# Performance work log

Measured on AMD Instinct MI355X. Metric: run time of the kernel, lower is better.

The kernel has to match this reference:

```python
import jax, jax.numpy as jnp
import numpy as np

NB_POOLS = 256


def setup_inputs() -> dict:
    key = jax.random.key(0)
    x = jax.random.normal(key, (32, 32, 32, 512), dtype=jnp.float32)
    return {"x": x}


def reference(x) -> jnp.ndarray:
    B, R, C, F = x.shape
    nb_maps = R * C
    x3 = x.reshape(B, nb_maps, F)
    # self-correlation: (B, nb_maps, nb_maps), normalized by feature count
    corr = jnp.einsum('bmf,bnf->bmn', x3, x3) / F
    corr = corr.reshape(B, R, C, nb_maps)
    # percentile ranks into the descending-sorted correlation values
    ranks = jnp.round(jnp.linspace(1.0, nb_maps - 1, NB_POOLS)).astype(jnp.int32)
    # full descending sort along last axis (matches tf.nn.top_k k=nb_maps)
    x_sort = -jnp.sort(-corr, axis=-1)
    x_pool = x_sort[..., ranks]  # (B, R, C, NB_POOLS)
    return x_pool
```

## Files before the change

kernel.cpp:

```cpp
#include <hip/hip_runtime.h>


#define NMAPS 1024
#define FDIM 512
#define TM 16
#define NT 256

typedef __attribute__((ext_vector_type(8))) short short8_t;
typedef __attribute__((ext_vector_type(4))) float f32x4;
typedef _Float16 h2 __attribute__((ext_vector_type(2)));

#define SELD 0x03020504u
#define SELA 0x07060100u

__device__ __forceinline__ h2 h2min(h2 a, h2 b) { return __builtin_elementwise_min(a, b); }
__device__ __forceinline__ h2 h2max(h2 a, h2 b) { return __builtin_elementwise_max(a, b); }

__device__ __forceinline__ unsigned h2u(h2 x) { union { h2 h; unsigned u; } t; t.h = x; return t.u; }
__device__ __forceinline__ h2 u2h(unsigned x) { union { h2 h; unsigned u; } t; t.u = x; return t.h; }

__device__ __forceinline__ h2 h2swap(h2 v) {
  unsigned u = h2u(v);
  return u2h((u >> 16) | (u << 16));
}

__device__ __forceinline__ h2 h2shfl_xor(h2 v, int m) {
  union { h2 h; int i; } u;
  u.h = v;
  u.i = __shfl_xor(u.i, m, 64);
  return u.h;
}

__device__ __forceinline__ void ce_pair(h2& a, h2& b, bool d) {
  h2 mn = h2min(a, b), mx = h2max(a, b);
  a = d ? mx : mn;
  b = d ? mn : mx;
}

__device__ __forceinline__ h2 ce1(h2 w, unsigned sel) {
  h2 s = h2swap(w);
  h2 mn = h2min(w, s), mx = h2max(w, s);
#if __has_builtin(__builtin_amdgcn_perm)
  return u2h(__builtin_amdgcn_perm(h2u(mx), h2u(mn), sel));
#else
  h2 rd; rd[0] = mx[0]; rd[1] = mn[1];
  h2 ra; ra[0] = mn[0]; ra[1] = mx[1];
  return (sel == SELD) ? rd : ra;
#endif
}

__device__ __forceinline__ void intra_merge16(h2 w[8], bool d, unsigned sel) {
  ce_pair(w[0], w[4], d); ce_pair(w[1], w[5], d); ce_pair(w[2], w[6], d); ce_pair(w[3], w[7], d);
  ce_pair(w[0], w[2], d); ce_pair(w[1], w[3], d); ce_pair(w[4], w[6], d); ce_pair(w[5], w[7], d);
  ce_pair(w[0], w[1], d); ce_pair(w[2], w[3], d); ce_pair(w[4], w[5], d); ce_pair(w[6], w[7], d);
#pragma unroll
  for (int u = 0; u < 8; ++u) w[u] = ce1(w[u], sel);
}

__device__ __forceinline__ void sort16(h2 w[8], bool d, unsigned sd, unsigned si) {
  w[0] = ce1(w[0], sd); w[1] = ce1(w[1], si); w[2] = ce1(w[2], sd); w[3] = ce1(w[3], si);
  w[4] = ce1(w[4], sd); w[5] = ce1(w[5], si); w[6] = ce1(w[6], sd); w[7] = ce1(w[7], si);
  ce_pair(w[0], w[1], d); ce_pair(w[2], w[3], !d); ce_pair(w[4], w[5], d); ce_pair(w[6], w[7], !d);
  w[0] = ce1(w[0], sd); w[1] = ce1(w[1], sd); w[2] = ce1(w[2], si); w[3] = ce1(w[3], si);
  w[4] = ce1(w[4], sd); w[5] = ce1(w[5], sd); w[6] = ce1(w[6], si); w[7] = ce1(w[7], si);
  ce_pair(w[0], w[2], d); ce_pair(w[1], w[3], d); ce_pair(w[4], w[6], !d); ce_pair(w[5], w[7], !d);
  ce_pair(w[0], w[1], d); ce_pair(w[2], w[3], d); ce_pair(w[4], w[5], !d); ce_pair(w[6], w[7], !d);
  w[0] = ce1(w[0], sd); w[1] = ce1(w[1], sd); w[2] = ce1(w[2], sd); w[3] = ce1(w[3], sd);
  w[4] = ce1(w[4], si); w[5] = ce1(w[5], si); w[6] = ce1(w[6], si); w[7] = ce1(w[7], si);
  intra_merge16(w, d, sd);
}

__device__ __forceinline__ void merge32(h2 w[16], bool d) {
  const unsigned sel = d ? SELD : SELA;
#pragma unroll
  for (int u = 0; u < 8; ++u) ce_pair(w[u], w[u + 8], d);
#pragma unroll
  for (int u = 0; u < 16; ++u)
    if ((u & 4) == 0) ce_pair(w[u], w[u | 4], d);
#pragma unroll
  for (int u = 0; u < 16; ++u)
    if ((u & 2) == 0) ce_pair(w[u], w[u | 2], d);
#pragma unroll
  for (int u = 0; u < 16; ++u)
    if ((u & 1) == 0) ce_pair(w[u], w[u | 1], d);
#pragma unroll
  for (int u = 0; u < 16; ++u) w[u] = ce1(w[u], sel);
}

template<int N>
__device__ __forceinline__ void cross_ceN(h2* w, int m, bool keepmax) {
#pragma unroll
  for (int u = 0; u < N; ++u) {
    h2 p = h2shfl_xor(w[u], m);
    h2 mn = h2min(w[u], p), mx = h2max(w[u], p);
    w[u] = keepmax ? mx : mn;
  }
}
__device__ __forceinline__ void cross_ce(h2 w[8], int m, bool keepmax) {
  cross_ceN<8>(w, m, keepmax);
}

template<int K>
__device__ __forceinline__ void bitonic_stage(h2 w8[8], int lane) {
  const bool laneDesc = (K >= 16) ? ((lane & (K >> 4)) == 0) : true;
#pragma unroll
  for (int j = 512; j >= 16; j >>= 1) {
    if (j > (K >> 1)) continue;
    const int m = j >> 4;
    const bool keepmax = (((lane & m) == 0) == laneDesc);
#pragma unroll
    for (int u = 0; u < 8; ++u) {
      h2 p = h2shfl_xor(w8[u], m);
      h2 mn = h2min(w8[u], p), mx = h2max(w8[u], p);
      w8[u] = keepmax ? mx : mn;
    }
  }
#pragma unroll
  for (int j = 8; j >= 2; j >>= 1) {
    if (j > (K >> 1)) continue;
    const int jw = j >> 1;
#pragma unroll
    for (int u = 0; u < 8; ++u) {
      if ((u & jw) == 0) {
        const int v = u | jw;
        const bool desc = (K <= 8) ? (((2 * u) & K) == 0) : laneDesc;
        h2 mn = h2min(w8[u], w8[v]), mx = h2max(w8[u], w8[v]);
        w8[u] = desc ? mx : mn;
        w8[v] = desc ? mn : mx;
      }
    }
  }
#pragma unroll
  for (int u = 0; u < 8; ++u) {
    const bool desc = (K <= 8) ? (((2 * u) & K) == 0) : laneDesc;
    h2 s = h2swap(w8[u]);
    h2 mn = h2min(w8[u], s), mx = h2max(w8[u], s);
    h2 rd = (h2){mx[0], mn[1]};
    h2 ra = (h2){mn[0], mx[1]};
    w8[u] = desc ? rd : ra;
  }
}

template<int K>
__device__ __forceinline__ void bitonic_stage_tail(h2 w8[8], int lane) {
  const bool laneDesc = ((lane & (K >> 4)) == 0);
#pragma unroll
  for (int j = 512; j >= 16; j >>= 1) {
    if (j > (K >> 1)) continue;
    const int m = j >> 4;
    cross_ce(w8, m, ((lane & m) == 0) == laneDesc);
  }
  intra_merge16(w8, laneDesc, laneDesc ? SELD : SELA);
}

__device__ __forceinline__ void run_bitonic(h2 w8[8], int lane) {
  bitonic_stage<2>(w8, lane);
  bitonic_stage<4>(w8, lane);
  bitonic_stage<8>(w8, lane);
  bitonic_stage<16>(w8, lane);
  bitonic_stage<32>(w8, lane);
  bitonic_stage<64>(w8, lane);
  bitonic_stage<128>(w8, lane);
  bitonic_stage<256>(w8, lane);
  bitonic_stage<512>(w8, lane);
  bitonic_stage<1024>(w8, lane);
}

__global__ __launch_bounds__(256) void cvt_bf16_kernel(const float* __restrict__ x,
                                                       short* __restrict__ xw, int n8) {
  int i = blockIdx.x * 256 + threadIdx.x;
  if (i >= n8) return;
  const float4* x4 = reinterpret_cast<const float4*>(x);
  float4 a = x4[i * 2], c = x4[i * 2 + 1];
  float f[8] = {a.x, a.y, a.z, a.w, c.x, c.y, c.z, c.w};
  union { short8_t v; short s[8]; } o;
#pragma unroll
  for (int j = 0; j < 8; ++j) {
    unsigned u = __float_as_uint(f[j]);
    u += 0x7fffu + ((u >> 16) & 1u);
    o.s[j] = (short)(u >> 16);
  }
  reinterpret_cast<short8_t*>(xw)[i] = o.v;
}

__global__ __launch_bounds__(512) void corr_gemm_tiled(const short* __restrict__ xw,
                                                       unsigned* __restrict__ corrW) {
  __shared__ short Asm[2][128 * 32];
  __shared__ short Bsm[2][128 * 32];
  const int tid = threadIdx.x;
  const int b = blockIdx.y;
  const int it = blockIdx.x >> 3, jt = blockIdx.x & 7;
  const int i0 = it * 128, j0 = jt * 128;
  const int lane = tid & 63;
  const int w = tid >> 6;
  const int lr = lane & 15;
  const int kg = lane >> 4;
  const short* Xb = xw + (size_t)b * NMAPS * FDIM;

  const int sr = tid >> 2;
  const int ss = (tid & 3) ^ ((sr >> 1) & 3);
  const int srcOff = sr * FDIM + ss * 8;
  const int dstOff = tid * 8;

  const int rowa = w * 16 + lr;
  const int aOff = rowa * 32 + (kg ^ ((rowa >> 1) & 3)) * 8;
  int bOff[8];
#pragma unroll
  for (int fn = 0; fn < 8; ++fn) {
    const int rowb = fn * 16 + lr;
    bOff[fn] = rowb * 32 + (kg ^ ((rowb >> 1) & 3)) * 8;
  }

  f32x4 acc[8];
#pragma unroll
  for (int fn = 0; fn < 8; ++fn) acc[fn] = (f32x4){0.f, 0.f, 0.f, 0.f};

#define STAGE(buf, kt)                                                                \
  {                                                                                   \
    const short* gA = Xb + (size_t)i0 * FDIM + srcOff + (kt) * 32;                    \
    const short* gB = Xb + (size_t)j0 * FDIM + srcOff + (kt) * 32;                    \
    __builtin_amdgcn_global_load_lds(                                                 \
        (const __attribute__((address_space(1))) unsigned*)gA,                        \
        (__attribute__((address_space(3))) unsigned*)(Asm[buf] + dstOff), 16, 0, 0);  \
    __builtin_amdgcn_global_load_lds(                                                 \
        (const __attribute__((address_space(1))) unsigned*)gB,                        \
        (__attribute__((address_space(3))) unsigned*)(Bsm[buf] + dstOff), 16, 0, 0);  \
  }

  STAGE(0, 0);
  __syncthreads();

  for (int kt = 0; kt < 16; ++kt) {
    const int cur = kt & 1;
    if (kt < 15) STAGE(cur ^ 1, kt + 1);

    short8_t a = *reinterpret_cast<const short8_t*>(Asm[cur] + aOff);
    short8_t bf[8];
#pragma unroll
    for (int fn = 0; fn < 8; ++fn)
      bf[fn] = *reinterpret_cast<const short8_t*>(Bsm[cur] + bOff[fn]);
#pragma unroll
    for (int fn = 0; fn < 8; ++fn)
      acc[fn] = __builtin_amdgcn_mfma_f32_16x16x32_bf16(bf[fn], a, acc[fn], 0, 0, 0);

    __syncthreads();
  }
#undef STAGE

  {
    const bool D128 = ((jt & 1) == 0);
    const bool d64 = ((kg & 2) == 0);
    const bool d32 = ((kg & 1) == 0);
    h2 W[16];
#pragma unroll
    for (int fn = 0; fn < 8; ++fn) {
      W[2 * fn] = (h2){(_Float16)acc[fn][0], (_Float16)acc[fn][1]};
      W[2 * fn + 1] = (h2){(_Float16)acc[fn][2], (_Float16)acc[fn][3]};
    }
    sort16(W, true, SELD, SELA);
    sort16(W + 8, false, SELA, SELD);
    merge32(W, d32);
    cross_ceN<16>(W, 16, d32 == d64);
    merge32(W, d64);
    cross_ceN<16>(W, 32, d64 == D128);
    cross_ceN<16>(W, 16, d32 == D128);
    merge32(W, D128);
    const size_t roww = ((size_t)b * NMAPS + i0 + w * 16 + lr) * 512;
    const int wq = (j0 >> 1) + kg * 16;
    union { h2 h[4]; uint4 u; } s0, s1, s2, s3;
#pragma unroll
    for (int q = 0; q < 4; ++q) { s0.h[q] = W[q]; s1.h[q] = W[4 + q]; s2.h[q] = W[8 + q]; s3.h[q] = W[12 + q]; }
    *reinterpret_cast<uint4*>(corrW + roww + wq) = s0.u;
    *reinterpret_cast<uint4*>(corrW + roww + wq + 4) = s1.u;
    *reinterpret_cast<uint4*>(corrW + roww + wq + 8) = s2.u;
    *reinterpret_cast<uint4*>(corrW + roww + wq + 12) = s3.u;
  }
}

__global__ __launch_bounds__(256) void sort_rows_kernel(const unsigned* __restrict__ corrW,
                                                        float* __restrict__ out) {
  const int tid = threadIdx.x;
  const int lane = tid & 63;
  const int row = blockIdx.x * 4 + (tid >> 6);
  const uint4* r4 = reinterpret_cast<const uint4*>(corrW + (size_t)row * 512);

  h2 w8[8];
  {
    union { uint4 u; h2 h[4]; } a, c;
    a.u = r4[lane * 2];
    c.u = r4[lane * 2 + 1];
    w8[0] = a.h[0]; w8[1] = a.h[1]; w8[2] = a.h[2]; w8[3] = a.h[3];
    w8[4] = c.h[0]; w8[5] = c.h[1]; w8[6] = c.h[2]; w8[7] = c.h[3];
  }

  bitonic_stage_tail<256>(w8, lane);
  bitonic_stage_tail<512>(w8, lane);
  bitonic_stage_tail<1024>(w8, lane);

  float* orow = out + (size_t)row * 256;
#pragma unroll
  for (int u = 0; u < 8; ++u) {
#pragma unroll
    for (int hh = 0; hh < 2; ++hh) {
      const int i = lane * 16 + 2 * u + hh;
      const int p = (int)rint((double)(i - 1) * (255.0 / 1022.0));
      const int rk = (int)rint(1.0 + (double)p * (1022.0 / 255.0));
      if (rk == i) orow[p] = (float)w8[u][hh] * (1.f / FDIM);
    }
  }
}

__global__ __launch_bounds__(NT) void selfcorr_mfma_kernel(const short* __restrict__ xw,
                                                           float* __restrict__ out) {
  __shared__ alignas(16) h2 SH[TM * 512];
  const int tid = threadIdx.x;
  const int b = blockIdx.y;
  const int m0 = blockIdx.x * TM;
  const int lane = tid & 63;
  const int wid = tid >> 6;
  const int lr = lane & 15;
  const int kg = lane >> 4;
  const int wc = wid * 256;
  const short* Xb = xw + (size_t)b * NMAPS * FDIM;

  f32x4 acc[16];
#pragma unroll
  for (int t = 0; t < 16; ++t) acc[t] = (f32x4){0.f, 0.f, 0.f, 0.f};

  for (int kk = 0; kk < 16; ++kk) {
    const short8_t* base = reinterpret_cast<const short8_t*>(Xb + kk * 32 + kg * 8);
    short8_t afrag = base[(size_t)(m0 + lr) * 64];
    short8_t bfrag[16];
#pragma unroll
    for (int t = 0; t < 16; ++t) bfrag[t] = base[(size_t)(wc + t * 16 + lr) * 64];
#pragma unroll
    for (int t = 0; t < 16; ++t)
      acc[t] = __builtin_amdgcn_mfma_f32_16x16x32_bf16(bfrag[t], afrag, acc[t], 0, 0, 0);
  }

  {
    const int xorv = (lr & 7) << 2;
#pragma unroll
    for (int t = 0; t < 16; ++t) {
      h2 lo = (h2){(_Float16)(acc[t][0] * (1.f / FDIM)), (_Float16)(acc[t][1] * (1.f / FDIM))};
      h2 hi = (h2){(_Float16)(acc[t][2] * (1.f / FDIM)), (_Float16)(acc[t][3] * (1.f / FDIM))};
      const int W = (wc >> 1) + t * 8 + kg * 2;
      const int phys = lr * 512 + (W ^ xorv);
      union { h2 h[2]; uint2 u; } pk;
      pk.h[0] = lo; pk.h[1] = hi;
      *reinterpret_cast<uint2*>(&SH[phys]) = pk.u;
    }
  }
  __syncthreads();

  const int rowbase = wid * 4;
  for (int rr = rowbase; rr < rowbase + 4; ++rr) {
    const int rx = (rr & 7) << 2;
    h2 w8[8];
#pragma unroll
    for (int q = 0; q < 2; ++q) {
      const int p4 = rr * 512 + ((lane * 8 + q * 4) ^ rx);
      union { uint4 u; h2 h[4]; } un;
      un.u = *reinterpret_cast<const uint4*>(&SH[p4]);
      w8[q * 4 + 0] = un.h[0]; w8[q * 4 + 1] = un.h[1];
      w8[q * 4 + 2] = un.h[2]; w8[q * 4 + 3] = un.h[3];
    }
    run_bitonic(w8, lane);
#pragma unroll
    for (int q = 0; q < 2; ++q) {
      const int p4 = rr * 512 + ((lane * 8 + q * 4) ^ rx);
      union { uint4 u; h2 h[4]; } un;
      un.h[0] = w8[q * 4 + 0]; un.h[1] = w8[q * 4 + 1];
      un.h[2] = w8[q * 4 + 2]; un.h[3] = w8[q * 4 + 3];
      *reinterpret_cast<uint4*>(&SH[p4]) = un.u;
    }
  }
  __builtin_amdgcn_wave_barrier();

#pragma unroll
  for (int i = 0; i < 16; ++i) {
    const int rr = rowbase + (i >> 2);
    const int p = lane + ((i & 3) << 6);
    const int rank = (int)rint(1.0 + (double)p * (1022.0 / 255.0));
    const int Wr = (rank >> 1) ^ ((rr & 7) << 2);
    h2 hv = SH[rr * 512 + Wr];
    out[((size_t)(b * NMAPS + m0 + rr) << 8) + p] = (float)hv[rank & 1];
  }
}

__device__ __forceinline__ int sw4(int row, int c4) {
  return (row << 8) | (c4 ^ ((c4 >> 3) & 7));
}
__device__ __forceinline__ void ce(float& a, float& b, bool desc) {
  float mn = fminf(a, b);
  float mx = fmaxf(a, b);
  a = desc ? mx : mn;
  b = desc ? mn : mx;
}

__global__ __launch_bounds__(NT) void selfcorr_pool_kernel(const float* __restrict__ x,
                                                           float* __restrict__ out) {
  __shared__ float lds[TM * NMAPS];
  float4* S4 = reinterpret_cast<float4*>(lds);
  const int tid = threadIdx.x;
  const int b = blockIdx.y;
  const int m0 = blockIdx.x * TM;
  const float4* Xb = reinterpret_cast<const float4*>(x) + (size_t)b * NMAPS * (FDIM / 4);

  float4* A4 = reinterpret_cast<float4*>(lds);
#pragma unroll
  for (int idx = tid; idx < TM * (FDIM / 4); idx += NT) {
    A4[idx] = Xb[(m0 + (idx >> 7)) * 128 + (idx & 127)];
  }
  __syncthreads();

  float acc[TM][4];
#pragma unroll
  for (int m = 0; m < TM; ++m)
#pragma unroll
    for (int j = 0; j < 4; ++j) acc[m][j] = 0.0f;

  float4 nb0 = Xb[(tid + 0) * 128];
  float4 nb1 = Xb[(tid + 256) * 128];
  float4 nb2 = Xb[(tid + 512) * 128];
  float4 nb3 = Xb[(tid + 768) * 128];
  for (int k4 = 0; k4 < 128; ++k4) {
    float4 b0 = nb0, b1 = nb1, b2 = nb2, b3 = nb3;
    const int kn = (k4 < 127) ? (k4 + 1) : 127;
    nb0 = Xb[(tid + 0) * 128 + kn];
    nb1 = Xb[(tid + 256) * 128 + kn];
    nb2 = Xb[(tid + 512) * 128 + kn];
    nb3 = Xb[(tid + 768) * 128 + kn];
#pragma unroll
    for (int m = 0; m < TM; ++m) {
      float4 a = A4[m * 128 + k4];
      acc[m][0] += a.x * b0.x + a.y * b0.y + a.z * b0.z + a.w * b0.w;
      acc[m][1] += a.x * b1.x + a.y * b1.y + a.z * b1.z + a.w * b1.w;
      acc[m][2] += a.x * b2.x + a.y * b2.y + a.z * b2.z + a.w * b2.w;
      acc[m][3] += a.x * b3.x + a.y * b3.y + a.z * b3.z + a.w * b3.w;
    }
  }
  __syncthreads();

#pragma unroll
  for (int m = 0; m < TM; ++m) {
#pragma unroll
    for (int j = 0; j < 4; ++j) {
      const int n = tid + (j << 8);
      lds[sw4(m, n >> 2) * 4 + (n & 3)] = acc[m][j] * (1.0f / FDIM);
    }
  }
  __syncthreads();

#pragma unroll
  for (int c = 0; c < 2; ++c) {
    const int cid = tid + (c << 8);
    const int row = cid >> 5;
    const int chunk = cid & 31;
    float r[32];
#pragma unroll
    for (int q = 0; q < 8; ++q) {
      float4 t = S4[sw4(row, (chunk << 3) + q)];
      r[q * 4 + 0] = t.x; r[q * 4 + 1] = t.y; r[q * 4 + 2] = t.z; r[q * 4 + 3] = t.w;
    }
    const bool D = ((chunk & 1) == 0);
#pragma unroll
    for (int k2 = 2; k2 <= 32; k2 <<= 1) {
#pragma unroll
      for (int j = k2 >> 1; j > 0; j >>= 1) {
#pragma unroll
        for (int i = 0; i < 32; ++i) {
          if ((i & j) == 0) ce(r[i], r[i | j], ((i & k2) == 0) ? D : !D);
        }
      }
    }
#pragma unroll
    for (int q = 0; q < 8; ++q) {
      S4[sw4(row, (chunk << 3) + q)] =
          make_float4(r[q * 4 + 0], r[q * 4 + 1], r[q * 4 + 2], r[q * 4 + 3]);
    }
  }
  __syncthreads();

  for (int k = 64; k <= NMAPS; k <<= 1) {
    for (int j = k >> 1; j >= 32; j >>= 1) {
      const int j4 = j >> 2;
      const int kq = k >> 2;
#pragma unroll
      for (int q = 0; q < 8; ++q) {
        const int g = tid + (q << 8);
        const int row = g >> 7;
        const int v = g & 127;
        const int i4 = ((v & ~(j4 - 1)) << 1) | (v & (j4 - 1));
        const bool desc = ((i4 & kq) == 0);
        const int ia = sw4(row, i4);
        const int ib = sw4(row, i4 + j4);
        float4 va = S4[ia];
        float4 vb = S4[ib];
        float4 lo, hi;
        lo.x = fminf(va.x, vb.x); hi.x = fmaxf(va.x, vb.x);
        lo.y = fminf(va.y, vb.y); hi.y = fmaxf(va.y, vb.y);
        lo.z = fminf(va.z, vb.z); hi.z = fmaxf(va.z, vb.z);
        lo.w = fminf(va.w, vb.w); hi.w = fmaxf(va.w, vb.w);
        S4[ia] = desc ? hi : lo;
        S4[ib] = desc ? lo : hi;
      }
      __syncthreads();
    }
#pragma unroll
    for (int c = 0; c < 2; ++c) {
      const int cid = tid + (c << 8);
      const int row = cid >> 5;
      const int chunk = cid & 31;
      const bool D = (((chunk << 5) & k) == 0);
      float r[32];
#pragma unroll
      for (int q = 0; q < 8; ++q) {
        float4 t = S4[sw4(row, (chunk << 3) + q)];
        r[q * 4 + 0] = t.x; r[q * 4 + 1] = t.y; r[q * 4 + 2] = t.z; r[q * 4 + 3] = t.w;
      }
#pragma unroll
      for (int j = 16; j > 0; j >>= 1) {
#pragma unroll
        for (int i = 0; i < 32; ++i) {
          if ((i & j) == 0) ce(r[i], r[i | j], D);
        }
      }
#pragma unroll
      for (int q = 0; q < 8; ++q) {
        S4[sw4(row, (chunk << 3) + q)] =
            make_float4(r[q * 4 + 0], r[q * 4 + 1], r[q * 4 + 2], r[q * 4 + 3]);
      }
    }
    __syncthreads();
  }

  const int p = tid;
  const int rank = (int)rint(1.0 + (double)p * (1022.0 / 255.0));
#pragma unroll
  for (int m = 0; m < TM; ++m) {
    out[((size_t)(b * NMAPS + m0 + m) << 8) + p] = lds[sw4(m, rank >> 2) * 4 + (rank & 3)];
  }
}

extern "C" void kernel_launch(void* const* d_in, const int* in_sizes, int n_in,
                              void* d_out, int out_size, void* d_ws, size_t ws_size,
                              hipStream_t stream) {
  const float* x = reinterpret_cast<const float*>(d_in[0]);
  float* out = reinterpret_cast<float*>(d_out);
  const int nelem = in_sizes[0];
  const int B = nelem / (NMAPS * FDIM);
  const size_t need_split = (size_t)nelem * 2 + (size_t)B * NMAPS * NMAPS * 2;
  if (ws_size >= need_split) {
    short* xw = reinterpret_cast<short*>(d_ws);
    unsigned* corrW = reinterpret_cast<unsigned*>((char*)d_ws + (size_t)nelem * 2);
    const int n8 = nelem / 8;
    hipLaunchKernelGGL(cvt_bf16_kernel, dim3((n8 + 255) / 256), dim3(256), 0, stream, x, xw, n8);
    hipLaunchKernelGGL(corr_gemm_tiled, dim3(64, B), dim3(512), 0, stream, xw, corrW);
    hipLaunchKernelGGL(sort_rows_kernel, dim3(B * NMAPS / 4), dim3(256), 0, stream, corrW, out);
  } else if (ws_size >= (size_t)nelem * 2) {
    short* xw = reinterpret_cast<short*>(d_ws);
    const int n8 = nelem / 8;
    hipLaunchKernelGGL(cvt_bf16_kernel, dim3((n8 + 255) / 256), dim3(256), 0, stream, x, xw, n8);
    hipLaunchKernelGGL(selfcorr_mfma_kernel, dim3(NMAPS / TM, B), dim3(NT), 0, stream, xw, out);
  } else {
    hipLaunchKernelGGL(selfcorr_pool_kernel, dim3(NMAPS / TM, B), dim3(NT), 0, stream, x, out);
  }
}
```

Before: 164.0 us.

## Remap GEMM blocks per XCD by batch and sort two rows per wave

The correlation GEMM moves to a 1D grid. When there are 2048 blocks, each batch's 64 tiles are remapped to land on the same XCD, so that batch's input stays in one XCD's L2. The row-sort kernel now has each wave process two rows in an interleaved way. This doubles independent work per wave, hiding shuffle and compare latency, and halves the block count. In exchange it uses more registers and relies on the assumption that blocks are dispatched round-robin across 8 XCDs.

New measurement: 161.2 us. No clear change (-1.7%).

```diff
diff --git a/kernel.cpp b/kernel.cpp
--- a/kernel.cpp
+++ b/kernel.cpp
@@ -142,15 +142,19 @@
 }
 
 template<int K>
-__device__ __forceinline__ void bitonic_stage_tail(h2 w8[8], int lane) {
+__device__ __forceinline__ void bitonic_stage_tail2(h2 A[8], h2 B[8], int lane) {
   const bool laneDesc = ((lane & (K >> 4)) == 0);
 #pragma unroll
   for (int j = 512; j >= 16; j >>= 1) {
     if (j > (K >> 1)) continue;
     const int m = j >> 4;
-    cross_ce(w8, m, ((lane & m) == 0) == laneDesc);
-  }
-  intra_merge16(w8, laneDesc, laneDesc ? SELD : SELA);
+    const bool km = (((lane & m) == 0) == laneDesc);
+    cross_ce(A, m, km);
+    cross_ce(B, m, km);
+  }
+  const unsigned sel = laneDesc ? SELD : SELA;
+  intra_merge16(A, laneDesc, sel);
+  intra_merge16(B, laneDesc, sel);
 }
 
 __device__ __forceinline__ void run_bitonic(h2 w8[8], int lane) {
@@ -188,8 +192,18 @@
   __shared__ short Asm[2][128 * 32];
   __shared__ short Bsm[2][128 * 32];
   const int tid = threadIdx.x;
-  const int b = blockIdx.y;
-  const int it = blockIdx.x >> 3, jt = blockIdx.x & 7;
+  int b, tile;
+  if (gridDim.x == 2048) {
+    const int bid = blockIdx.x;
+    const int xcd = bid & 7;
+    const int j = bid >> 3;
+    b = (j >> 6) * 8 + xcd;
+    tile = j & 63;
+  } else {
+    b = blockIdx.x >> 6;
+    tile = blockIdx.x & 63;
+  }
+  const int it = tile >> 3, jt = tile & 7;
   const int i0 = it * 128, j0 = jt * 128;
   const int lane = tid & 63;
   const int w = tid >> 6;
@@ -281,23 +295,28 @@
                                                         float* __restrict__ out) {
   const int tid = threadIdx.x;
   const int lane = tid & 63;
-  const int row = blockIdx.x * 4 + (tid >> 6);
-  const uint4* r4 = reinterpret_cast<const uint4*>(corrW + (size_t)row * 512);
-
-  h2 w8[8];
+  const int rA = blockIdx.x * 8 + (tid >> 6) * 2;
+  const int rB = rA + 1;
+  const uint4* pa = reinterpret_cast<const uint4*>(corrW + (size_t)rA * 512);
+  const uint4* pb = reinterpret_cast<const uint4*>(corrW + (size_t)rB * 512);
+
+  h2 A[8], B[8];
   {
-    union { uint4 u; h2 h[4]; } a, c;
-    a.u = r4[lane * 2];
-    c.u = r4[lane * 2 + 1];
-    w8[0] = a.h[0]; w8[1] = a.h[1]; w8[2] = a.h[2]; w8[3] = a.h[3];
-    w8[4] = c.h[0]; w8[5] = c.h[1]; w8[6] = c.h[2]; w8[7] = c.h[3];
-  }
-
-  bitonic_stage_tail<256>(w8, lane);
-  bitonic_stage_tail<512>(w8, lane);
-  bitonic_stage_tail<1024>(w8, lane);
-
-  float* orow = out + (size_t)row * 256;
+    union { uint4 u; h2 h[4]; } t0, t1;
+    t0.u = pa[lane * 2]; t1.u = pa[lane * 2 + 1];
+    A[0] = t0.h[0]; A[1] = t0.h[1]; A[2] = t0.h[2]; A[3] = t0.h[3];
+    A[4] = t1.h[0]; A[5] = t1.h[1]; A[6] = t1.h[2]; A[7] = t1.h[3];
+    t0.u = pb[lane * 2]; t1.u = pb[lane * 2 + 1];
+    B[0] = t0.h[0]; B[1] = t0.h[1]; B[2] = t0.h[2]; B[3] = t0.h[3];
+    B[4] = t1.h[0]; B[5] = t1.h[1]; B[6] = t1.h[2]; B[7] = t1.h[3];
+  }
+
+  bitonic_stage_tail2<256>(A, B, lane);
+  bitonic_stage_tail2<512>(A, B, lane);
+  bitonic_stage_tail2<1024>(A, B, lane);
+
+  float* oa = out + (size_t)rA * 256;
+  float* ob = out + (size_t)rB * 256;
 #pragma unroll
   for (int u = 0; u < 8; ++u) {
 #pragma unroll
@@ -305,7 +324,10 @@
       const int i = lane * 16 + 2 * u + hh;
       const int p = (int)rint((double)(i - 1) * (255.0 / 1022.0));
       const int rk = (int)rint(1.0 + (double)p * (1022.0 / 255.0));
-      if (rk == i) orow[p] = (float)w8[u][hh] * (1.f / FDIM);
+      if (rk == i) {
+        oa[p] = (float)A[u][hh] * (1.f / FDIM);
+        ob[p] = (float)B[u][hh] * (1.f / FDIM);
+      }
     }
   }
 }
@@ -556,8 +578,8 @@
     unsigned* corrW = reinterpret_cast<unsigned*>((char*)d_ws + (size_t)nelem * 2);
     const int n8 = nelem / 8;
     hipLaunchKernelGGL(cvt_bf16_kernel, dim3((n8 + 255) / 256), dim3(256), 0, stream, x, xw, n8);
-    hipLaunchKernelGGL(corr_gemm_tiled, dim3(64, B), dim3(512), 0, stream, xw, corrW);
-    hipLaunchKernelGGL(sort_rows_kernel, dim3(B * NMAPS / 4), dim3(256), 0, stream, corrW, out);
+    hipLaunchKernelGGL(corr_gemm_tiled, dim3(64 * B), dim3(512), 0, stream, xw, corrW);
+    hipLaunchKernelGGL(sort_rows_kernel, dim3(B * NMAPS / 8), dim3(256), 0, stream, corrW, out);
   } else if (ws_size >= (size_t)nelem * 2) {
     short* xw = reinterpret_cast<short*>(d_ws);
     const int n8 = nelem / 8;
```
